# Kernel optimization log

Measured on AMD Instinct MI355X. Metric: run time of the kernel, lower is better.

## Reference

```python
import jax, jax.numpy as jnp
import numpy as np


def _rope(v):
    # v: (B, S, H). Faithful to the torch RotaryEmbedding, including its
    # emb = cat(sin, cos) followed by emb[..., ::2]/[..., 1::2] slicing.
    B, S, H = v.shape
    inv_freq = 1.0 / (10000.0 ** (jnp.arange(0, H, 2, dtype=jnp.float32) / H))  # (H/2,)
    t = jnp.arange(S, dtype=jnp.float32)
    freqs = t[:, None] * inv_freq[None, :]                       # (S, H/2)
    emb = jnp.concatenate([jnp.sin(freqs), jnp.cos(freqs)], -1)  # (S, H)
    x1, x2 = v[..., ::2], v[..., 1::2]                           # (B, S, H/2) each
    emb_sin, emb_cos = emb[..., ::2], emb[..., 1::2]             # (S, H/2) each
    return jnp.concatenate([x1 * emb_cos - x2 * emb_sin,
                            x1 * emb_sin + x2 * emb_cos], -1)


def setup_inputs() -> dict:
    key = jax.random.key(0)
    ks = jax.random.split(key, 9)
    B, S, H = 2, 2048, 512
    sc = 0.02
    return {
        "x": jax.random.normal(ks[0], (B, S, H), dtype=jnp.float32),
        "Wq": jax.random.normal(ks[1], (H, H), dtype=jnp.float32) * sc,
        "bq": jax.random.normal(ks[2], (H,), dtype=jnp.float32) * sc,
        "Wk": jax.random.normal(ks[3], (H, H), dtype=jnp.float32) * sc,
        "bk": jax.random.normal(ks[4], (H,), dtype=jnp.float32) * sc,
        "Wv": jax.random.normal(ks[5], (H, H), dtype=jnp.float32) * sc,
        "bv": jax.random.normal(ks[6], (H,), dtype=jnp.float32) * sc,
        "Wo": jax.random.normal(ks[7], (H, H), dtype=jnp.float32) * sc,
        "bo": jax.random.normal(ks[8], (H,), dtype=jnp.float32) * sc,
    }


WINDOW_SIZE = 128


def reference(x, Wq, bq, Wk, bk, Wv, bv, Wo, bo):
    B, S, H = x.shape
    W = WINDOW_SIZE
    pad = W // 2
    # Projections (torch Linear: x @ W.T + b)
    Q = x @ Wq.T + bq
    K = x @ Wk.T + bk
    V = x @ Wv.T + bv
    rQ = _rope(Q)
    rK = _rope(K)
    # Pad along seq and gather sliding windows: window t covers positions t-pad .. t+pad-1
    pK = jnp.pad(rK, ((0, 0), (pad, pad), (0, 0)))
    pV = jnp.pad(V, ((0, 0), (pad, pad), (0, 0)))
    idx = jnp.arange(S)[:, None] + jnp.arange(W)[None, :]  # (S, W) into padded seq
    Kw = pK[:, idx, :]  # (B, S, W, H)
    Vw = pV[:, idx, :]  # (B, S, W, H)
    scores = jnp.einsum("bth,btwh->btw", rQ, Kw) / jnp.sqrt(jnp.float32(H))
    weights = jax.nn.softmax(scores, axis=-1)
    out = jnp.einsum("btw,btwh->bth", weights, Vw)
    return out @ Wo.T + bo
```

## Files before the change

### kernel.cpp

```cpp
#include <hip/hip_runtime.h>
#include <math.h>

#define S_LEN 2048
#define B_SZ  2
#define H_DIM 512
#define WIN   128
#define PAD   64
#define SP    (S_LEN + WIN)
#define SCALE 0.044194173824159216f
#define TQ    32

typedef __bf16 bf16;
typedef __attribute__((ext_vector_type(8))) __bf16 bf16x8;
typedef __attribute__((ext_vector_type(4))) __bf16 bf16x4;
typedef __attribute__((ext_vector_type(4))) float f32x4;

#define GLDS16(g, l) __builtin_amdgcn_global_load_lds( \
    (const __attribute__((address_space(1))) void*)(g), \
    (__attribute__((address_space(3))) void*)(l), 16, 0, 0)

__global__ __launch_bounds__(256) void prep_k(
    const float* __restrict__ x,
    const float* __restrict__ Wq, const float* __restrict__ Wk,
    const float* __restrict__ Wv, const float* __restrict__ Wo,
    bf16* __restrict__ xb, bf16* __restrict__ wb,
    bf16* __restrict__ pKb, bf16* __restrict__ pVT,
    float* __restrict__ sinT, float* __restrict__ cosT)
{
  int i = blockIdx.x * 256 + threadIdx.x;
  if (i < 262144) {
    int e = i * 8;
    float4 v0 = *(const float4*)(x + e);
    float4 v1 = *(const float4*)(x + e + 4);
    bf16x8 o = {(bf16)v0.x, (bf16)v0.y, (bf16)v0.z, (bf16)v0.w,
                (bf16)v1.x, (bf16)v1.y, (bf16)v1.z, (bf16)v1.w};
    *(bf16x8*)(xb + e) = o;
  } else if (i < 524288) {
    int idx = (i - 262144) * 4;
    int m = idx >> 18;
    const float* src = (m == 0) ? Wq : (m == 1) ? Wk : (m == 2) ? Wv : Wo;
    float4 v = *(const float4*)(src + (idx & 262143));
    bf16x4 hv = {(bf16)v.x, (bf16)v.y, (bf16)v.z, (bf16)v.w};
    *(bf16x4*)(wb + idx) = hv;
  } else if (i < 557056) {
    int idx = i - 524288;
    float4 z = {0.f, 0.f, 0.f, 0.f};
    if (idx < 16384) {
      int b = idx >> 13, r = (idx & 8191) >> 6, c = idx & 63;
      int row = (r < 64) ? r : (S_LEN + r);
      *(float4*)(pKb + ((size_t)b * SP + row) * 512 + c * 8) = z;
    } else {
      int j = idx - 16384;
      int b = j >> 13, h = (j & 8191) >> 4, v = j & 15;
      int col = (v < 8) ? v * 8 : (S_LEN + PAD + (v - 8) * 8);
      *(float4*)(pVT + ((size_t)b * 512 + h) * SP + col) = z;
    }
  } else {
    int idx = i - 557056;
    int s = idx >> 7, jj = idx & 127;
    float fqA = exp2f(-(float)jj * 0.10381025296523f);
    float fqB = exp2f(-(float)(2 * jj + 1) * 0.05190512648262f);
    float aA = (float)s * fqA;
    float aB = (float)s * fqB;
    sinT[s * 256 + jj]       = sinf(aA);
    sinT[s * 256 + jj + 128] = cosf(aA);
    cosT[s * 256 + jj]       = sinf(aB);
    cosT[s * 256 + jj + 128] = cosf(aB);
  }
}

template<int MFR, int MODE>
__global__ __launch_bounds__(256) void gemm_k(
    const bf16* __restrict__ Ab, const bf16* __restrict__ Wb,
    const float* __restrict__ bq, const float* __restrict__ bk,
    const float* __restrict__ bv,
    const float* __restrict__ sinT, const float* __restrict__ cosT,
    bf16* __restrict__ oQ, bf16* __restrict__ oK, bf16* __restrict__ oVT,
    float* __restrict__ oOut)
{
  constexpr int BM = MFR * 32;
  constexpr int ABYTES = BM * 128;
  constexpr int BUFB = ABYTES + 128 * 128;
  __shared__ __align__(16) unsigned char smem[2 * BUFB];
  const int tid = threadIdx.x;
  const int lane = tid & 63, wid = tid >> 6;
  const int wm = wid >> 1, wn = wid & 1;
  const int row0 = blockIdx.x * BM;
  const int wrow0 = (MODE == 0 ? 0 : 1536) + blockIdx.y * 128;
  const int lr = lane & 15, lk = lane >> 4;

  f32x4 acc[MFR][4] = {};

  auto stage = [&](int k0, int bufsel) {
    unsigned char* buf = smem + bufsel * BUFB;
#pragma unroll
    for (int i = 0; i < MFR; i++) {
      int c = tid + i * 256;
      int r = c >> 3, p = c & 7, l = p ^ (r & 7);
      GLDS16(Ab + (size_t)(row0 + r) * 512 + k0 + l * 8, buf + c * 16);
    }
#pragma unroll
    for (int j = 0; j < 4; j++) {
      int c = tid + j * 256;
      int r = c >> 3, p = c & 7, l = p ^ (r & 7);
      GLDS16(Wb + (size_t)(wrow0 + r) * 512 + k0 + l * 8, buf + ABYTES + c * 16);
    }
  };

  stage(0, 0);
  __syncthreads();
  for (int t = 0; t < 8; t++) {
    if (t < 7) stage((t + 1) * 64, (t + 1) & 1);
    const unsigned char* buf = smem + (t & 1) * BUFB;
    bf16x8 bfr[4][2];
#pragma unroll
    for (int ni = 0; ni < 4; ni++) {
      int r = wn * 64 + ni * 16 + lr;
      const unsigned char* base = buf + ABYTES + r * 128;
      int sw = (r & 7) << 4;
      bfr[ni][0] = *(const bf16x8*)(base + ((lk * 16) ^ sw));
      bfr[ni][1] = *(const bf16x8*)(base + ((64 + lk * 16) ^ sw));
    }
#pragma unroll
    for (int mi = 0; mi < MFR; mi++) {
      int r = wm * (MFR * 16) + mi * 16 + lr;
      const unsigned char* base = buf + r * 128;
      int sw = (r & 7) << 4;
      bf16x8 a0 = *(const bf16x8*)(base + ((lk * 16) ^ sw));
      bf16x8 a1 = *(const bf16x8*)(base + ((64 + lk * 16) ^ sw));
#pragma unroll
      for (int ni = 0; ni < 4; ni++) {
        acc[mi][ni] = __builtin_amdgcn_mfma_f32_16x16x32_bf16(a0, bfr[ni][0], acc[mi][ni], 0, 0, 0);
        acc[mi][ni] = __builtin_amdgcn_mfma_f32_16x16x32_bf16(a1, bfr[ni][1], acc[mi][ni], 0, 0, 0);
      }
    }
    __syncthreads();
  }

  const int rowb = row0 + wm * (MFR * 16) + ((lane >> 4) * 4);
  if (MODE == 1) {
#pragma unroll
    for (int mi = 0; mi < MFR; mi++)
#pragma unroll
      for (int ni = 0; ni < 4; ni++) {
        int col = blockIdx.y * 128 + wn * 64 + ni * 16 + (lane & 15);
        float bb = bq[col];
#pragma unroll
        for (int g = 0; g < 4; g++) {
          int rr = rowb + mi * 16 + g;
          oOut[(size_t)rr * 512 + col] = acc[mi][ni][g] + bb;
        }
      }
    return;
  }
  const int region = blockIdx.y >> 2;
  const float* bias = (region == 0) ? bq : (region == 1) ? bk : bv;
  const int cm0 = (blockIdx.y & 3) * 128;
#pragma unroll
  for (int mi = 0; mi < MFR; mi++)
#pragma unroll
    for (int ni = 0; ni < 4; ni++) {
      int c = cm0 + wn * 64 + ni * 16 + (lane & 15);
      float bb = bias[c];
      if (region == 2) {
#pragma unroll
        for (int g = 0; g < 4; g++) {
          int rr = rowb + mi * 16 + g;
          int b = rr >> 11, s = rr & 2047;
          oVT[((size_t)b * 512 + c) * SP + PAD + s] = (bf16)(acc[mi][ni][g] + bb);
        }
      } else {
        int j = c >> 1, par = c & 1;
#pragma unroll
        for (int g = 0; g < 4; g++) {
          int rr = rowb + mi * 16 + g;
          int s = rr & 2047;
          float v = acc[mi][ni][g] + bb;
          float p = __shfl_xor(v, 1);
          float es = sinT[s * 256 + j], ec = cosT[s * 256 + j];
          float res = par ? (p * es + v * ec) : (v * ec - p * es);
          int oc = par ? (j + 256) : j;
          if (region == 0) oQ[(size_t)rr * 512 + oc] = (bf16)res;
          else { int b = rr >> 11; oK[((size_t)b * SP + PAD + s) * 512 + oc] = (bf16)res; }
        }
      }
    }
}

__global__ __launch_bounds__(256) void attn_mfma_k(
    const bf16* __restrict__ rQb, const bf16* __restrict__ pKb,
    const bf16* __restrict__ pVT, bf16* __restrict__ ab)
{
  __shared__ __align__(16) unsigned char smem[53760];
  const int tid = threadIdx.x, lane = tid & 63, w = tid >> 6;
  const int q0g = blockIdx.x * TQ;
  const int nbase = blockIdx.y * 256;
  const int b = q0g >> 11, s0 = q0g & 2047;
  const int lr = lane & 15, lk = lane >> 4;
  const int OFF_K = 8192, OFF_P = 43008;

  f32x4 sacc[5] = {};
  const int tm = w >> 1, tnb = (w & 1) * 5;

  auto stageQK = [&](int k0, int sel) {
    {
      int r = tid >> 3, p = tid & 7, l = p ^ (r & 7);
      GLDS16(rQb + (size_t)(q0g + r) * 512 + k0 + l * 8,
             smem + sel * 4096 + tid * 16);
    }
#pragma unroll
    for (int i = 0; i < 5; i++) {
      int c = tid + i * 256;
      int r = c >> 3, p = c & 7, l = p ^ (r & 7);
      GLDS16(pKb + ((size_t)b * SP + s0 + r) * 512 + k0 + l * 8,
             smem + OFF_K + sel * 20480 + c * 16);
    }
  };

  stageQK(0, 0);
  __syncthreads();
  for (int t = 0; t < 8; t++) {
    if (t < 7) stageQK((t + 1) * 64, (t + 1) & 1);
    const unsigned char* qb = smem + (t & 1) * 4096;
    const unsigned char* kb = smem + OFF_K + (t & 1) * 20480;
    __builtin_amdgcn_s_setprio(1);
#pragma unroll
    for (int kk = 0; kk < 2; kk++) {
      int arow = tm * 16 + lr;
      bf16x8 a = *(const bf16x8*)(qb + arow * 128 + (((kk * 64 + lk * 16) ^ ((arow & 7) << 4))));
#pragma unroll
      for (int i = 0; i < 5; i++) {
        int brow = (tnb + i) * 16 + lr;
        bf16x8 bb = *(const bf16x8*)(kb + brow * 128 + (((kk * 64 + lk * 16) ^ ((brow & 7) << 4))));
        sacc[i] = __builtin_amdgcn_mfma_f32_16x16x32_bf16(a, bb, sacc[i], 0, 0, 0);
      }
    }
    __builtin_amdgcn_s_setprio(0);
    __syncthreads();
  }
  {
    float* sc = (float*)smem;
#pragma unroll
    for (int i = 0; i < 5; i++) {
      int col = (tnb + i) * 16 + lr;
#pragma unroll
      for (int g = 0; g < 4; g++) {
        int row = tm * 16 + lk * 4 + g;
        sc[row * 164 + col] = sacc[i][g] * SCALE;
      }
    }
  }
  __syncthreads();
  {
    float* sc = (float*)smem;
    bf16* P = (bf16*)(smem + OFF_P);
    int row = tid >> 3, j0 = tid & 7;
    float vals[20];
    float mx = -1e30f;
#pragma unroll
    for (int i = 0; i < 20; i++) {
      int j = j0 + i * 8;
      bool valid = (j >= row) && (j <= row + 127);
      float v = valid ? sc[row * 164 + j] : -1e30f;
      vals[i] = v;
      mx = fmaxf(mx, v);
    }
#pragma unroll
    for (int off = 1; off < 8; off <<= 1) mx = fmaxf(mx, __shfl_xor(mx, off));
    float sum = 0.f;
#pragma unroll
    for (int i = 0; i < 20; i++) {
      float e = (vals[i] > -1e29f) ? __expf(vals[i] - mx) : 0.f;
      vals[i] = e; sum += e;
    }
#pragma unroll
    for (int off = 1; off < 8; off <<= 1) sum += __shfl_xor(sum, off);
    float inv = 1.f / sum;
#pragma unroll
    for (int i = 0; i < 20; i++) {
      int j = j0 + i * 8;
      P[row * 168 + j] = (bf16)(vals[i] * inv);
    }
  }
  const bf16* pVTb = pVT + (size_t)b * 512 * SP;
  const int utm = w >> 1, utnb = (w & 1) * 4;
  for (int n0 = nbase; n0 < nbase + 256; n0 += 128) {
    __syncthreads();
    {
      int r = tid >> 1, half = tid & 1;
      const bf16* src = pVTb + (size_t)(n0 + r) * SP + s0;
#pragma unroll
      for (int i = 0; i < 10; i++) {
        int slot = half * 10 + i;
        float4 v = *(const float4*)(src + slot * 8);
        *(float4*)(smem + r * 336 + slot * 16) = v;
      }
    }
    __syncthreads();
    f32x4 oacc[4] = {};
    __builtin_amdgcn_s_setprio(1);
#pragma unroll
    for (int tk = 0; tk < 5; tk++) {
      int arow = utm * 16 + lr;
      bf16x8 a = *(const bf16x8*)(smem + OFF_P + arow * 336 + tk * 64 + lk * 16);
#pragma unroll
      for (int i = 0; i < 4; i++) {
        int brow = (utnb + i) * 16 + lr;
        bf16x8 bb = *(const bf16x8*)(smem + brow * 336 + tk * 64 + lk * 16);
        oacc[i] = __builtin_amdgcn_mfma_f32_16x16x32_bf16(a, bb, oacc[i], 0, 0, 0);
      }
    }
    __builtin_amdgcn_s_setprio(0);
#pragma unroll
    for (int i = 0; i < 4; i++) {
      int col = n0 + (utnb + i) * 16 + lr;
#pragma unroll
      for (int g = 0; g < 4; g++) {
        int row = utm * 16 + lk * 4 + g;
        ab[(size_t)(q0g + row) * 512 + col] = (bf16)oacc[i][g];
      }
    }
  }
}

extern "C" void kernel_launch(void* const* d_in, const int* in_sizes, int n_in,
                              void* d_out, int out_size, void* d_ws, size_t ws_size,
                              hipStream_t stream) {
  const float* x  = (const float*)d_in[0];
  const float* Wq = (const float*)d_in[1];
  const float* bq = (const float*)d_in[2];
  const float* Wk = (const float*)d_in[3];
  const float* bk = (const float*)d_in[4];
  const float* Wv = (const float*)d_in[5];
  const float* bv = (const float*)d_in[6];
  const float* Wo = (const float*)d_in[7];
  const float* bo = (const float*)d_in[8];
  float* out = (float*)d_out;

  const size_t NQ = (size_t)B_SZ * S_LEN * H_DIM;
  const size_t NP = (size_t)B_SZ * SP * H_DIM;
  float* sinT = (float*)d_ws;
  float* cosT = sinT + (size_t)S_LEN * 256;
  bf16* xb  = (bf16*)(cosT + (size_t)S_LEN * 256);
  bf16* wb  = xb + NQ;
  bf16* rQb = wb + 2048 * 512;
  bf16* pKb = rQb + NQ;
  bf16* pVT = pKb + NP;
  bf16* ab  = pVT + NP;

  prep_k<<<3200, 256, 0, stream>>>(x, Wq, Wk, Wv, Wo, xb, wb,
                                   pKb, pVT, sinT, cosT);

  gemm_k<4, 0><<<dim3(32, 12), 256, 0, stream>>>(xb, wb,
      bq, bk, bv, sinT, cosT, rQb, pKb, pVT, nullptr);

  attn_mfma_k<<<dim3(B_SZ * S_LEN / TQ, 2), 256, 0, stream>>>(rQb, pKb, pVT, ab);

  gemm_k<2, 1><<<dim3(64, 4), 256, 0, stream>>>(ab, wb,
      bo, nullptr, nullptr, sinT, cosT, nullptr, nullptr, nullptr, out);
}
```

Before: 47.60 us.

## Split attention QK reduction across two warp groups with 512-thread blocks

Doubles the attention block to 512 threads. Two 4-wave groups each compute half of the 512-wide head dimension for the QK^T scores into separate shared buffers, and the softmax sums the two partials. The PV stage and softmax work are spread over 8 waves instead of 4. This aims to cut the serial K-loop length per block and raise parallelism. In exchange, shared memory per block grows to 96KB, which can lower occupancy, and it adds an extra partial-sum pass.

```diff
diff --git a/kernel.cpp b/kernel.cpp
--- a/kernel.cpp
+++ b/kernel.cpp
@@ -187,42 +187,44 @@
     }
 }
 
-__global__ __launch_bounds__(256) void attn_mfma_k(
+__global__ __launch_bounds__(512) void attn_mfma_k(
     const bf16* __restrict__ rQb, const bf16* __restrict__ pKb,
     const bf16* __restrict__ pVT, bf16* __restrict__ ab)
 {
-  __shared__ __align__(16) unsigned char smem[53760];
+  __shared__ __align__(16) unsigned char smem[98304];
   const int tid = threadIdx.x, lane = tid & 63, w = tid >> 6;
+  const int g = w >> 2, ww = w & 3, gtid = tid & 255;
   const int q0g = blockIdx.x * TQ;
   const int nbase = blockIdx.y * 256;
   const int b = q0g >> 11, s0 = q0g & 2047;
   const int lr = lane & 15, lk = lane >> 4;
-  const int OFF_K = 8192, OFF_P = 43008;
+  const int GB = g * 49152;
+  const int OFF_P = 43008;
 
   f32x4 sacc[5] = {};
-  const int tm = w >> 1, tnb = (w & 1) * 5;
+  const int tm = ww >> 1, tnb = (ww & 1) * 5;
 
   auto stageQK = [&](int k0, int sel) {
     {
-      int r = tid >> 3, p = tid & 7, l = p ^ (r & 7);
+      int r = gtid >> 3, p = gtid & 7, l = p ^ (r & 7);
       GLDS16(rQb + (size_t)(q0g + r) * 512 + k0 + l * 8,
-             smem + sel * 4096 + tid * 16);
+             smem + GB + sel * 4096 + gtid * 16);
     }
 #pragma unroll
     for (int i = 0; i < 5; i++) {
-      int c = tid + i * 256;
+      int c = gtid + i * 256;
       int r = c >> 3, p = c & 7, l = p ^ (r & 7);
       GLDS16(pKb + ((size_t)b * SP + s0 + r) * 512 + k0 + l * 8,
-             smem + OFF_K + sel * 20480 + c * 16);
+             smem + GB + 8192 + sel * 20480 + c * 16);
     }
   };
 
-  stageQK(0, 0);
+  stageQK(g * 256, 0);
   __syncthreads();
-  for (int t = 0; t < 8; t++) {
-    if (t < 7) stageQK((t + 1) * 64, (t + 1) & 1);
-    const unsigned char* qb = smem + (t & 1) * 4096;
-    const unsigned char* kb = smem + OFF_K + (t & 1) * 20480;
+  for (int t = 0; t < 4; t++) {
+    if (t < 3) stageQK(g * 256 + (t + 1) * 64, (t + 1) & 1);
+    const unsigned char* qb = smem + GB + (t & 1) * 4096;
+    const unsigned char* kb = smem + GB + 8192 + (t & 1) * 20480;
     __builtin_amdgcn_s_setprio(1);
 #pragma unroll
     for (int kk = 0; kk < 2; kk++) {
@@ -239,72 +241,70 @@
     __syncthreads();
   }
   {
-    float* sc = (float*)smem;
+    float* sc = (float*)(smem + g * 21504);
 #pragma unroll
     for (int i = 0; i < 5; i++) {
       int col = (tnb + i) * 16 + lr;
 #pragma unroll
-      for (int g = 0; g < 4; g++) {
-        int row = tm * 16 + lk * 4 + g;
-        sc[row * 164 + col] = sacc[i][g] * SCALE;
+      for (int gg = 0; gg < 4; gg++) {
+        int row = tm * 16 + lk * 4 + gg;
+        sc[row * 164 + col] = sacc[i][gg];
       }
     }
   }
   __syncthreads();
   {
-    float* sc = (float*)smem;
+    const float* sA = (const float*)smem;
+    const float* sB = (const float*)(smem + 21504);
     bf16* P = (bf16*)(smem + OFF_P);
-    int row = tid >> 3, j0 = tid & 7;
-    float vals[20];
+    int row = tid >> 4, j0 = tid & 15;
+    float vals[10];
     float mx = -1e30f;
 #pragma unroll
-    for (int i = 0; i < 20; i++) {
-      int j = j0 + i * 8;
+    for (int i = 0; i < 10; i++) {
+      int j = j0 + i * 16;
       bool valid = (j >= row) && (j <= row + 127);
-      float v = valid ? sc[row * 164 + j] : -1e30f;
+      float v = valid ? (sA[row * 164 + j] + sB[row * 164 + j]) * SCALE : -1e30f;
       vals[i] = v;
       mx = fmaxf(mx, v);
     }
 #pragma unroll
-    for (int off = 1; off < 8; off <<= 1) mx = fmaxf(mx, __shfl_xor(mx, off));
+    for (int off = 1; off < 16; off <<= 1) mx = fmaxf(mx, __shfl_xor(mx, off));
     float sum = 0.f;
 #pragma unroll
-    for (int i = 0; i < 20; i++) {
+    for (int i = 0; i < 10; i++) {
       float e = (vals[i] > -1e29f) ? __expf(vals[i] - mx) : 0.f;
       vals[i] = e; sum += e;
     }
 #pragma unroll
-    for (int off = 1; off < 8; off <<= 1) sum += __shfl_xor(sum, off);
+    for (int off = 1; off < 16; off <<= 1) sum += __shfl_xor(sum, off);
     float inv = 1.f / sum;
 #pragma unroll
-    for (int i = 0; i < 20; i++) {
-      int j = j0 + i * 8;
-      P[row * 168 + j] = (bf16)(vals[i] * inv);
-    }
+    for (int i = 0; i < 10; i++)
+      P[row * 168 + j0 + i * 16] = (bf16)(vals[i] * inv);
   }
   const bf16* pVTb = pVT + (size_t)b * 512 * SP;
-  const int utm = w >> 1, utnb = (w & 1) * 4;
+  const int utm = w >> 2, utnb = (w & 3) * 2;
   for (int n0 = nbase; n0 < nbase + 256; n0 += 128) {
     __syncthreads();
     {
-      int r = tid >> 1, half = tid & 1;
+      int r = tid >> 2, q = tid & 3;
       const bf16* src = pVTb + (size_t)(n0 + r) * SP + s0;
 #pragma unroll
-      for (int i = 0; i < 10; i++) {
-        int slot = half * 10 + i;
+      for (int i = 0; i < 5; i++) {
+        int slot = q * 5 + i;
         float4 v = *(const float4*)(src + slot * 8);
         *(float4*)(smem + r * 336 + slot * 16) = v;
       }
     }
     __syncthreads();
-    f32x4 oacc[4] = {};
+    f32x4 oacc[2] = {};
     __builtin_amdgcn_s_setprio(1);
 #pragma unroll
     for (int tk = 0; tk < 5; tk++) {
-      int arow = utm * 16 + lr;
-      bf16x8 a = *(const bf16x8*)(smem + OFF_P + arow * 336 + tk * 64 + lk * 16);
-#pragma unroll
-      for (int i = 0; i < 4; i++) {
+      bf16x8 a = *(const bf16x8*)(smem + OFF_P + (utm * 16 + lr) * 336 + tk * 64 + lk * 16);
+#pragma unroll
+      for (int i = 0; i < 2; i++) {
         int brow = (utnb + i) * 16 + lr;
         bf16x8 bb = *(const bf16x8*)(smem + brow * 336 + tk * 64 + lk * 16);
         oacc[i] = __builtin_amdgcn_mfma_f32_16x16x32_bf16(a, bb, oacc[i], 0, 0, 0);
@@ -312,12 +312,12 @@
     }
     __builtin_amdgcn_s_setprio(0);
 #pragma unroll
-    for (int i = 0; i < 4; i++) {
+    for (int i = 0; i < 2; i++) {
       int col = n0 + (utnb + i) * 16 + lr;
 #pragma unroll
-      for (int g = 0; g < 4; g++) {
-        int row = utm * 16 + lk * 4 + g;
-        ab[(size_t)(q0g + row) * 512 + col] = (bf16)oacc[i][g];
+      for (int gg = 0; gg < 4; gg++) {
+        int row = utm * 16 + lk * 4 + gg;
+        ab[(size_t)(q0g + row) * 512 + col] = (bf16)oacc[i][gg];
       }
     }
   }
@@ -354,7 +354,7 @@
   gemm_k<4, 0><<<dim3(32, 12), 256, 0, stream>>>(xb, wb,
       bq, bk, bv, sinT, cosT, rQb, pKb, pVT, nullptr);
 
-  attn_mfma_k<<<dim3(B_SZ * S_LEN / TQ, 2), 256, 0, stream>>>(rQb, pKb, pVT, ab);
+  attn_mfma_k<<<dim3(B_SZ * S_LEN / TQ, 2), 512, 0, stream>>>(rQb, pKb, pVT, ab);
 
   gemm_k<2, 1><<<dim3(64, 4), 256, 0, stream>>>(ab, wb,
       bo, nullptr, nullptr, sinT, cosT, nullptr, nullptr, nullptr, out);
```

Result: faster. 46.00 us (-3.4%).
